# Optimization experiments

Hardware: AMD Instinct MI355X
Metric: run time of the kernel (lower is better)

The kernel has to match this reference:

```python
import jax, jax.numpy as jnp
import numpy as np

B, S, H, I, E, K = 2, 512, 512, 1024, 64, 4


def setup_inputs() -> dict:
    key = jax.random.key(0)
    ks = jax.random.split(key, 16)
    scale = jnp.float32(0.02)

    def w(k, shape):
        return jax.random.normal(k, shape, dtype=jnp.float32) * scale

    return {
        "x": jax.random.normal(ks[0], (B, S, H), dtype=jnp.float32),
        "router_w": w(ks[1], (E, H)),
        "router_b": w(ks[2], (E,)),
        "expert_biases": jnp.zeros((E,), dtype=jnp.float32),
        "sw1": w(ks[3], (I, H)), "sb1": w(ks[4], (I,)),
        "sw2": w(ks[5], (H, I)), "sb2": w(ks[6], (H,)),
        "sw3": w(ks[7], (I, H)), "sb3": w(ks[8], (I,)),
        "w1": w(ks[9], (E, I, H)), "b1": w(ks[10], (E, I)),
        "w2": w(ks[11], (E, H, I)), "b2": w(ks[12], (E, H)),
        "w3": w(ks[13], (E, I, H)), "b3": w(ks[14], (E, I)),
        "top_k": K,
    }


def _ffn(x, w1, b1, w2, b2, w3, b3):
    return (jax.nn.silu(x @ w1.T + b1) * (x @ w3.T + b3)) @ w2.T + b2


def reference(x, router_w, router_b, expert_biases,
              sw1, sb1, sw2, sb2, sw3, sb3,
              w1, b1, w2, b2, w3, b3, top_k):
    Bx, Sx, Hx = x.shape
    Ex = router_w.shape[0]

    # Router: logits [B,S,E]; top-k selection uses bias-adjusted logits,
    # but gates come from the ORIGINAL (unbiased) logits.
    logits = x @ router_w.T + router_b
    _, idx = jax.lax.top_k(logits + expert_biases, top_k)  # [B,S,K] int32
    orig = jnp.take_along_axis(logits, idx, axis=-1)       # [B,S,K]
    scores = jax.nn.sigmoid(orig)
    gates = scores / jnp.maximum(jnp.sum(scores, axis=-1, keepdims=True), 1e-12)

    # Shared expert(s): num_shared_experts == 1, divided by 1.
    shared = _ffn(x, sw1, sb1, sw2, sb2, sw3, sb3)

    # Combine gates into a dense per-token per-expert gate matrix [T,E].
    xf = x.reshape(-1, Hx)                 # [T,H]
    T = xf.shape[0]
    tok = jnp.arange(T)[:, None]
    gate_full = jnp.zeros((T, Ex), x.dtype).at[tok, idx.reshape(T, top_k)].add(
        gates.reshape(T, top_k))

    # Routed experts: each expert FFN over all tokens, gated combine.
    # (Mathematically identical to the original masked-dense loop: the mask
    #  zeroes both inputs and gates of unassigned tokens.)
    def body(acc, p):
        ew1, eb1, ew2, eb2, ew3, eb3, g = p
        y = _ffn(xf, ew1, eb1, ew2, eb2, ew3, eb3)  # [T,H]
        return acc + g[:, None] * y, None

    acc, _ = jax.lax.scan(body, jnp.zeros_like(xf),
                          (w1, b1, w2, b2, w3, b3, gate_full.T))

    return shared + acc.reshape(x.shape)
```

## Files before the change

### kernel.cpp

```cpp
#include <hip/hip_runtime.h>
#include <math.h>

#define T_    1024
#define H_    512
#define I_    1024
#define E_    64
#define K_    4
#define NPAIR (T_*K_)
#define NENT  (NPAIR + T_)

#define BM 128
#define BN 64
#define BKS 64
#define MAXWORK 160
#define NT1 (H_/BKS)
#define NT2 (I_/BKS)

typedef float  f32x4  __attribute__((ext_vector_type(4)));
typedef short  bf16x8 __attribute__((ext_vector_type(8)));

__device__ __forceinline__ ushort f2bf(float f) {
    uint u = __float_as_uint(f);
    u += 0x7fffu + ((u >> 16) & 1u);
    return (ushort)(u >> 16);
}
__device__ __forceinline__ bf16x8 cvt8(f32x4 a, f32x4 b) {
    bf16x8 r;
    r[0] = (short)f2bf(a[0]); r[1] = (short)f2bf(a[1]);
    r[2] = (short)f2bf(a[2]); r[3] = (short)f2bf(a[3]);
    r[4] = (short)f2bf(b[0]); r[5] = (short)f2bf(b[1]);
    r[6] = (short)f2bf(b[2]); r[7] = (short)f2bf(b[3]);
    return r;
}

__device__ __forceinline__ void gload16(const void* g, void* lds) {
    __builtin_amdgcn_global_load_lds(
        (const __attribute__((address_space(1))) unsigned int*)g,
        (__attribute__((address_space(3))) unsigned int*)lds, 16, 0, 0);
}

__global__ __launch_bounds__(256) void x_cvt(const float* __restrict__ x,
                                             ushort* __restrict__ xb)
{
    const int i = blockIdx.x*256 + threadIdx.x;
    float4 v = reinterpret_cast<const float4*>(x)[i];
    reinterpret_cast<ushort4*>(xb)[i] =
        make_ushort4(f2bf(v.x), f2bf(v.y), f2bf(v.z), f2bf(v.w));
}

__global__ __launch_bounds__(64) void moe_router(
    const float* __restrict__ x, const float* __restrict__ rw,
    const float* __restrict__ rb, const float* __restrict__ eb,
    int* __restrict__ idx_out, float* __restrict__ gate_out)
{
    const int t = blockIdx.x;
    const int lane = threadIdx.x;
    __shared__ float xs[H_];
    __shared__ float lg[E_];
    __shared__ float bs[E_];
    for (int i = lane; i < H_; i += 64) xs[i] = x[(size_t)t*H_ + i];
    bs[lane] = eb[lane];
    __syncthreads();
    float acc = 0.f;
    const float* wrow = rw + (size_t)lane*H_;
    for (int k = 0; k < H_; k += 4) {
        float4 w4 = *reinterpret_cast<const float4*>(wrow + k);
        acc = fmaf(xs[k+0], w4.x, acc);
        acc = fmaf(xs[k+1], w4.y, acc);
        acc = fmaf(xs[k+2], w4.z, acc);
        acc = fmaf(xs[k+3], w4.w, acc);
    }
    lg[lane] = acc + rb[lane];
    __syncthreads();
    if (lane == 0) {
        unsigned long long used = 0ull;
        int sel[K_]; float orig[K_];
        for (int k = 0; k < K_; ++k) {
            float best = -INFINITY; int bi = 0;
            for (int e = 0; e < E_; ++e) {
                if (used & (1ull << e)) continue;
                float v = lg[e] + bs[e];
                if (v > best) { best = v; bi = e; }
            }
            used |= (1ull << bi);
            sel[k] = bi; orig[k] = lg[bi];
        }
        float s[K_]; float sum = 0.f;
        for (int k = 0; k < K_; ++k) { s[k] = 1.f/(1.f + __expf(-orig[k])); sum += s[k]; }
        sum = fmaxf(sum, 1e-12f);
        for (int k = 0; k < K_; ++k) {
            idx_out[t*K_ + k] = sel[k];
            gate_out[t*K_ + k] = s[k] / sum;
        }
    }
}

__global__ __launch_bounds__(256) void moe_build(
    const int* __restrict__ idx, const float* __restrict__ gates,
    int* __restrict__ cnts, int* __restrict__ offs,
    int* __restrict__ entry_token, float* __restrict__ entry_gate,
    int* __restrict__ pair_pos,
    int* __restrict__ blk_e, int* __restrict__ blk_ro, int* __restrict__ nwork)
{
    __shared__ int c[E_];
    __shared__ int run[E_];
    const int tid = threadIdx.x;
    if (tid < E_) c[tid] = 0;
    __syncthreads();
    for (int p = tid; p < NPAIR; p += 256) atomicAdd(&c[idx[p]], 1);
    __syncthreads();
    if (tid == 0) {
        int o = 0;
        for (int e = 0; e < E_; ++e) { run[e] = o; offs[e] = o; cnts[e] = c[e]; o += c[e]; }
        offs[E_] = NPAIR;
        cnts[E_] = T_;
        int nb = 0;
        for (int e = 0; e <= E_; ++e) {
            int n = (e < E_) ? c[e] : T_;
            for (int ro = 0; ro < n; ro += BM) { blk_e[nb] = e; blk_ro[nb] = ro; ++nb; }
        }
        nwork[0] = nb;
    }
    __syncthreads();
    for (int p = tid; p < NPAIR; p += 256) {
        int e = idx[p];
        int pos = atomicAdd(&run[e], 1);
        entry_token[pos] = p / K_;
        entry_gate[pos]  = gates[p];
        pair_pos[p]      = pos;
    }
    for (int t = tid; t < T_; t += 256) {
        entry_token[NPAIR + t] = t;
        entry_gate[NPAIR + t]  = 1.0f;
    }
}

__global__ __launch_bounds__(256, 3) void moe_stage1(
    const ushort* __restrict__ xbf,
    const float* __restrict__ w1, const float* __restrict__ b1,
    const float* __restrict__ w3, const float* __restrict__ b3,
    const float* __restrict__ sw1, const float* __restrict__ sb1,
    const float* __restrict__ sw3, const float* __restrict__ sb3,
    const int* __restrict__ cnts, const int* __restrict__ offs,
    const int* __restrict__ entry_token,
    const int* __restrict__ blk_e, const int* __restrict__ blk_ro,
    const int* __restrict__ nwork,
    ushort* __restrict__ h1buf)
{
    const int w = blockIdx.x;
    if (w >= nwork[0]) return;
    const int e  = blk_e[w];
    const int ro = blk_ro[w];
    const int itile = blockIdx.y;
    const int n = cnts[e];
    const int off = offs[e];
    const int rows = min(BM, n - ro);
    const float* W1 = (e < E_) ? (w1 + (size_t)e*I_*H_) : sw1;
    const float* W3 = (e < E_) ? (w3 + (size_t)e*I_*H_) : sw3;
    const float* B1 = (e < E_) ? (b1 + (size_t)e*I_) : sb1;
    const float* B3 = (e < E_) ? (b3 + (size_t)e*I_) : sb3;

    __shared__ __align__(16) ushort XL [BM*BKS];
    __shared__ __align__(16) float  W1L[BN*BKS];
    __shared__ __align__(16) float  W3L[BN*BKS];

    const int tid  = threadIdx.x;
    const int lane = tid & 63;
    const int wid  = tid >> 6;
    const int wm   = wid >> 1;
    const int wn   = wid & 1;
    const int l15  = lane & 15;
    const int lg   = lane >> 4;

    const ushort* xsrc[4];
    const float* w1src[4];
    const float* w3src[4];
    #pragma unroll
    for (int i = 0; i < 4; ++i) {
        const int j = wid*4 + i;
        const int rX = j*8 + (lane >> 3);
        const int cX = (lane & 7) ^ (rX & 7);
        xsrc[i] = xbf + (size_t)entry_token[off + ro + rX]*H_ + cX*8;
        const int rW = j*4 + (lane >> 4);
        const int c32 = ((lane & 15) >> 1) ^ (rW & 7);
        const int colW = c32*8 + (lane & 1)*4;
        w1src[i] = W1 + (size_t)(itile*BN + rW)*H_ + colW;
        w3src[i] = W3 + (size_t)(itile*BN + rW)*H_ + colW;
    }

    f32x4 acc1[4][2] = {};
    f32x4 acc3[4][2] = {};

    for (int t = 0; t < NT1; ++t) {
        const int kc = t * BKS;
        #pragma unroll
        for (int i = 0; i < 4; ++i)
            gload16(xsrc[i] + kc, (char*)XL + (wid*4 + i)*1024);
        #pragma unroll
        for (int i = 0; i < 4; ++i)
            gload16(w1src[i] + kc, (char*)W1L + (wid*4 + i)*1024);
        #pragma unroll
        for (int i = 0; i < 4; ++i)
            gload16(w3src[i] + kc, (char*)W3L + (wid*4 + i)*1024);
        __syncthreads();
        #pragma unroll
        for (int s = 0; s < 2; ++s) {
            bf16x8 a[4];
            #pragma unroll
            for (int fm = 0; fm < 4; ++fm) {
                const int rr = wm*64 + fm*16 + l15;
                a[fm] = *reinterpret_cast<const bf16x8*>(
                    (const char*)XL + rr*128 + (((s*4 + lg) ^ (rr & 7)) << 4));
            }
            bf16x8 b1f[2], b3f[2];
            #pragma unroll
            for (int fn = 0; fn < 2; ++fn) {
                const int rw = wn*32 + fn*16 + l15;
                const int cw = ((s*4 + lg) ^ (rw & 7)) << 5;
                const char* p1 = (const char*)W1L + rw*256 + cw;
                b1f[fn] = cvt8(*reinterpret_cast<const f32x4*>(p1),
                               *reinterpret_cast<const f32x4*>(p1 + 16));
                const char* p3 = (const char*)W3L + rw*256 + cw;
                b3f[fn] = cvt8(*reinterpret_cast<const f32x4*>(p3),
                               *reinterpret_cast<const f32x4*>(p3 + 16));
            }
            #pragma unroll
            for (int fm = 0; fm < 4; ++fm) {
                #pragma unroll
                for (int fn = 0; fn < 2; ++fn) {
                    acc1[fm][fn] = __builtin_amdgcn_mfma_f32_16x16x32_bf16(a[fm], b1f[fn], acc1[fm][fn], 0, 0, 0);
                    acc3[fm][fn] = __builtin_amdgcn_mfma_f32_16x16x32_bf16(a[fm], b3f[fn], acc3[fm][fn], 0, 0, 0);
                }
            }
        }
        __syncthreads();
    }

    #pragma unroll
    for (int fm = 0; fm < 4; ++fm) {
        #pragma unroll
        for (int fn = 0; fn < 2; ++fn) {
            const int col = itile*BN + wn*32 + fn*16 + l15;
            const float bv1 = B1[col];
            const float bv3 = B3[col];
            #pragma unroll
            for (int j = 0; j < 4; ++j) {
                const int rl = wm*64 + fm*16 + lg*4 + j;
                if (rl < rows) {
                    float z1 = acc1[fm][fn][j] + bv1;
                    float z3 = acc3[fm][fn][j] + bv3;
                    float h = z1 / (1.f + __expf(-z1)) * z3;
                    h1buf[(size_t)(off+ro+rl)*I_ + col] = f2bf(h);
                }
            }
        }
    }
}

__global__ __launch_bounds__(256, 4) void moe_stage2(
    const ushort* __restrict__ h1buf,
    const float* __restrict__ w2, const float* __restrict__ b2,
    const float* __restrict__ sw2, const float* __restrict__ sb2,
    const int* __restrict__ cnts, const int* __restrict__ offs,
    const float* __restrict__ entry_gate,
    const int* __restrict__ blk_e, const int* __restrict__ blk_ro,
    const int* __restrict__ nwork,
    float* __restrict__ ybuf)
{
    const int w = blockIdx.x;
    if (w >= nwork[0]) return;
    const int e  = blk_e[w];
    const int ro = blk_ro[w];
    const int htile = blockIdx.y;
    const int n = cnts[e];
    const int off = offs[e];
    const int rows = min(BM, n - ro);
    const float* W2 = (e < E_) ? (w2 + (size_t)e*H_*I_) : sw2;
    const float* B2 = (e < E_) ? (b2 + (size_t)e*H_) : sb2;

    __shared__ __align__(16) ushort HL [BM*BKS];
    __shared__ __align__(16) float  W2L[BN*BKS];

    const int tid  = threadIdx.x;
    const int lane = tid & 63;
    const int wid  = tid >> 6;
    const int wm   = wid >> 1;
    const int wn   = wid & 1;
    const int l15  = lane & 15;
    const int lg   = lane >> 4;

    const ushort* hsrc[4];
    const float*  wsrc[4];
    #pragma unroll
    for (int i = 0; i < 4; ++i) {
        const int j = wid*4 + i;
        const int rH = j*8 + (lane >> 3);
        const int cH = (lane & 7) ^ (rH & 7);
        hsrc[i] = h1buf + (size_t)(off + ro + rH)*I_ + cH*8;
        const int rW = j*4 + (lane >> 4);
        const int c32 = ((lane & 15) >> 1) ^ (rW & 7);
        wsrc[i] = W2 + (size_t)(htile*BN + rW)*I_ + c32*8 + (lane & 1)*4;
    }

    f32x4 acc[4][2] = {};

    for (int t = 0; t < NT2; ++t) {
        const int kc = t * BKS;
        #pragma unroll
        for (int i = 0; i < 4; ++i)
            gload16(hsrc[i] + kc, (char*)HL + (wid*4 + i)*1024);
        #pragma unroll
        for (int i = 0; i < 4; ++i)
            gload16(wsrc[i] + kc, (char*)W2L + (wid*4 + i)*1024);
        __syncthreads();
        #pragma unroll
        for (int s = 0; s < 2; ++s) {
            bf16x8 a[4];
            #pragma unroll
            for (int fm = 0; fm < 4; ++fm) {
                const int rr = wm*64 + fm*16 + l15;
                a[fm] = *reinterpret_cast<const bf16x8*>(
                    (const char*)HL + rr*128 + (((s*4 + lg) ^ (rr & 7)) << 4));
            }
            bf16x8 bf[2];
            #pragma unroll
            for (int fn = 0; fn < 2; ++fn) {
                const int rw = wn*32 + fn*16 + l15;
                const char* p = (const char*)W2L + rw*256 + (((s*4 + lg) ^ (rw & 7)) << 5);
                bf[fn] = cvt8(*reinterpret_cast<const f32x4*>(p),
                              *reinterpret_cast<const f32x4*>(p + 16));
            }
            #pragma unroll
            for (int fm = 0; fm < 4; ++fm) {
                #pragma unroll
                for (int fn = 0; fn < 2; ++fn) {
                    acc[fm][fn] = __builtin_amdgcn_mfma_f32_16x16x32_bf16(a[fm], bf[fn], acc[fm][fn], 0, 0, 0);
                }
            }
        }
        __syncthreads();
    }

    #pragma unroll
    for (int fm = 0; fm < 4; ++fm) {
        #pragma unroll
        for (int fn = 0; fn < 2; ++fn) {
            const int col = htile*BN + wn*32 + fn*16 + l15;
            const float bv = B2[col];
            #pragma unroll
            for (int j = 0; j < 4; ++j) {
                const int rl = wm*64 + fm*16 + lg*4 + j;
                if (rl < rows) {
                    const float g = entry_gate[off + ro + rl];
                    ybuf[(size_t)(off+ro+rl)*H_ + col] = (acc[fm][fn][j] + bv) * g;
                }
            }
        }
    }
}

__global__ __launch_bounds__(128) void moe_combine(
    const float* __restrict__ ybuf, const int* __restrict__ pair_pos,
    float* __restrict__ out)
{
    const int t = blockIdx.x;
    const int lane = threadIdx.x;
    const int h = lane * 4;
    const int p0 = pair_pos[t*K_+0], p1 = pair_pos[t*K_+1];
    const int p2 = pair_pos[t*K_+2], p3 = pair_pos[t*K_+3];
    float4 a  = *reinterpret_cast<const float4*>(ybuf + (size_t)(NPAIR+t)*H_ + h);
    float4 v0 = *reinterpret_cast<const float4*>(ybuf + (size_t)p0*H_ + h);
    float4 v1 = *reinterpret_cast<const float4*>(ybuf + (size_t)p1*H_ + h);
    float4 v2 = *reinterpret_cast<const float4*>(ybuf + (size_t)p2*H_ + h);
    float4 v3 = *reinterpret_cast<const float4*>(ybuf + (size_t)p3*H_ + h);
    float4 r;
    r.x = a.x + v0.x + v1.x + v2.x + v3.x;
    r.y = a.y + v0.y + v1.y + v2.y + v3.y;
    r.z = a.z + v0.z + v1.z + v2.z + v3.z;
    r.w = a.w + v0.w + v1.w + v2.w + v3.w;
    *reinterpret_cast<float4*>(out + (size_t)t*H_ + h) = r;
}

extern "C" void kernel_launch(void* const* d_in, const int* in_sizes, int n_in,
                              void* d_out, int out_size, void* d_ws, size_t ws_size,
                              hipStream_t stream)
{
    const float* x   = (const float*)d_in[0];
    const float* rw  = (const float*)d_in[1];
    const float* rb  = (const float*)d_in[2];
    const float* eb  = (const float*)d_in[3];
    const float* sw1 = (const float*)d_in[4];
    const float* sb1 = (const float*)d_in[5];
    const float* sw2 = (const float*)d_in[6];
    const float* sb2 = (const float*)d_in[7];
    const float* sw3 = (const float*)d_in[8];
    const float* sb3 = (const float*)d_in[9];
    const float* w1  = (const float*)d_in[10];
    const float* b1  = (const float*)d_in[11];
    const float* w2  = (const float*)d_in[12];
    const float* b2  = (const float*)d_in[13];
    const float* w3  = (const float*)d_in[14];
    const float* b3  = (const float*)d_in[15];
    float* out = (float*)d_out;

    char* p = (char*)d_ws;
    auto take = [&](size_t bytes) { char* q = p; p += (bytes + 255) & ~(size_t)255; return q; };
    int*    idxb  = (int*)   take((size_t)NPAIR*4);
    float*  gateb = (float*) take((size_t)NPAIR*4);
    int*    cnts  = (int*)   take((E_+1)*4);
    int*    offs  = (int*)   take((E_+1)*4);
    int*    etok  = (int*)   take((size_t)NENT*4);
    float*  egate = (float*) take((size_t)NENT*4);
    int*    ppos  = (int*)   take((size_t)NPAIR*4);
    int*    blk_e = (int*)   take((size_t)MAXWORK*4);
    int*    blk_ro= (int*)   take((size_t)MAXWORK*4);
    int*    nwork = (int*)   take(4);
    ushort* xbf   = (ushort*)take((size_t)T_*H_*2);
    ushort* h1buf = (ushort*)take((size_t)NENT*I_*2);
    float*  ybuf  = (float*) take((size_t)NENT*H_*4);

    x_cvt      <<<(T_*H_)/(256*4), 256, 0, stream>>>(x, xbf);
    moe_router <<<T_, 64, 0, stream>>>(x, rw, rb, eb, idxb, gateb);
    moe_build  <<<1, 256, 0, stream>>>(idxb, gateb, cnts, offs, etok, egate, ppos,
                                       blk_e, blk_ro, nwork);
    moe_stage1 <<<dim3(MAXWORK, I_/BN), 256, 0, stream>>>(xbf, w1, b1, w3, b3,
                                                          sw1, sb1, sw3, sb3,
                                                          cnts, offs, etok,
                                                          blk_e, blk_ro, nwork, h1buf);
    moe_stage2 <<<dim3(MAXWORK, H_/BN), 256, 0, stream>>>(h1buf, w2, b2, sw2, sb2,
                                                          cnts, offs, egate,
                                                          blk_e, blk_ro, nwork, ybuf);
    moe_combine<<<T_, 128, 0, stream>>>(ybuf, ppos, out);
}
```

Measured before the change: 201.7 us.

## Double-buffer LDS tiles in expert GEMMs with halved K-step and packed bf16 convert

Both expert GEMM kernels now keep two LDS buffers and issue the async global-to-LDS loads for the next K-step before computing on the current one. This lets memory latency overlap with the MFMAs instead of stalling at a barrier on every iteration. To keep LDS usage the same, the K-step is halved from 64 to 32, which doubles the number of iterations and barriers; the XOR swizzle and load addressing are rewritten for the narrower tile. The per-element software fp32-to-bf16 rounding is replaced with the hardware v_cvt_pk_bf16_f32 instruction, which cuts VALU work when converting the weight fragments.

```diff
diff --git a/kernel.cpp b/kernel.cpp
--- a/kernel.cpp
+++ b/kernel.cpp
@@ -11,26 +11,28 @@
 
 #define BM 128
 #define BN 64
-#define BKS 64
+#define BKS 32
 #define MAXWORK 160
 #define NT1 (H_/BKS)
 #define NT2 (I_/BKS)
 
 typedef float  f32x4  __attribute__((ext_vector_type(4)));
 typedef short  bf16x8 __attribute__((ext_vector_type(8)));
+
+#define STEP_SYNC() asm volatile("s_waitcnt vmcnt(0) lgkmcnt(0)\n\ts_barrier" ::: "memory")
 
 __device__ __forceinline__ ushort f2bf(float f) {
     uint u = __float_as_uint(f);
     u += 0x7fffu + ((u >> 16) & 1u);
     return (ushort)(u >> 16);
 }
-__device__ __forceinline__ bf16x8 cvt8(f32x4 a, f32x4 b) {
-    bf16x8 r;
-    r[0] = (short)f2bf(a[0]); r[1] = (short)f2bf(a[1]);
-    r[2] = (short)f2bf(a[2]); r[3] = (short)f2bf(a[3]);
-    r[4] = (short)f2bf(b[0]); r[5] = (short)f2bf(b[1]);
-    r[6] = (short)f2bf(b[2]); r[7] = (short)f2bf(b[3]);
-    return r;
+__device__ __forceinline__ bf16x8 cvt8pk(f32x4 a, f32x4 b) {
+    union { uint u[4]; bf16x8 v; } r;
+    asm("v_cvt_pk_bf16_f32 %0, %1, %2" : "=v"(r.u[0]) : "v"(a[0]), "v"(a[1]));
+    asm("v_cvt_pk_bf16_f32 %0, %1, %2" : "=v"(r.u[1]) : "v"(a[2]), "v"(a[3]));
+    asm("v_cvt_pk_bf16_f32 %0, %1, %2" : "=v"(r.u[2]) : "v"(b[0]), "v"(b[1]));
+    asm("v_cvt_pk_bf16_f32 %0, %1, %2" : "=v"(r.u[3]) : "v"(b[2]), "v"(b[3]));
+    return r.v;
 }
 
 __device__ __forceinline__ void gload16(const void* g, void* lds) {
@@ -160,9 +162,9 @@
     const float* B1 = (e < E_) ? (b1 + (size_t)e*I_) : sb1;
     const float* B3 = (e < E_) ? (b3 + (size_t)e*I_) : sb3;
 
-    __shared__ __align__(16) ushort XL [BM*BKS];
-    __shared__ __align__(16) float  W1L[BN*BKS];
-    __shared__ __align__(16) float  W3L[BN*BKS];
+    __shared__ __align__(16) ushort XL [2][BM*BKS];
+    __shared__ __align__(16) float  W1L[2][BN*BKS];
+    __shared__ __align__(16) float  W3L[2][BN*BKS];
 
     const int tid  = threadIdx.x;
     const int lane = tid & 63;
@@ -172,69 +174,73 @@
     const int l15  = lane & 15;
     const int lg   = lane >> 4;
 
-    const ushort* xsrc[4];
-    const float* w1src[4];
-    const float* w3src[4];
+    const ushort* xsrc[2];
+    const float* w1src[2];
+    const float* w3src[2];
     #pragma unroll
-    for (int i = 0; i < 4; ++i) {
-        const int j = wid*4 + i;
-        const int rX = j*8 + (lane >> 3);
-        const int cX = (lane & 7) ^ (rX & 7);
+    for (int i = 0; i < 2; ++i) {
+        const int j = wid*2 + i;
+        const int rX = j*16 + (lane >> 2);
+        const int cX = (lane & 3) ^ ((rX >> 1) & 3);
         xsrc[i] = xbf + (size_t)entry_token[off + ro + rX]*H_ + cX*8;
-        const int rW = j*4 + (lane >> 4);
-        const int c32 = ((lane & 15) >> 1) ^ (rW & 7);
-        const int colW = c32*8 + (lane & 1)*4;
-        w1src[i] = W1 + (size_t)(itile*BN + rW)*H_ + colW;
-        w3src[i] = W3 + (size_t)(itile*BN + rW)*H_ + colW;
+        const int rW = j*8 + (lane >> 3);
+        const int cW = (lane & 7) ^ (rW & 7);
+        w1src[i] = W1 + (size_t)(itile*BN + rW)*H_ + cW*4;
+        w3src[i] = W3 + (size_t)(itile*BN + rW)*H_ + cW*4;
     }
 
     f32x4 acc1[4][2] = {};
     f32x4 acc3[4][2] = {};
 
+    #define STAGE1(t, buf)                                                        \
+        do {                                                                      \
+            const int kc_ = (t) * BKS;                                            \
+            _Pragma("unroll")                                                     \
+            for (int i_ = 0; i_ < 2; ++i_) {                                      \
+                gload16(xsrc[i_] + kc_,  (char*)&XL [buf][0] + (wid*2 + i_)*1024);\
+                gload16(w1src[i_] + kc_, (char*)&W1L[buf][0] + (wid*2 + i_)*1024);\
+                gload16(w3src[i_] + kc_, (char*)&W3L[buf][0] + (wid*2 + i_)*1024);\
+            }                                                                     \
+        } while (0)
+
+    STAGE1(0, 0);
+    STEP_SYNC();
+
     for (int t = 0; t < NT1; ++t) {
-        const int kc = t * BKS;
-        #pragma unroll
-        for (int i = 0; i < 4; ++i)
-            gload16(xsrc[i] + kc, (char*)XL + (wid*4 + i)*1024);
-        #pragma unroll
-        for (int i = 0; i < 4; ++i)
-            gload16(w1src[i] + kc, (char*)W1L + (wid*4 + i)*1024);
-        #pragma unroll
-        for (int i = 0; i < 4; ++i)
-            gload16(w3src[i] + kc, (char*)W3L + (wid*4 + i)*1024);
-        __syncthreads();
-        #pragma unroll
-        for (int s = 0; s < 2; ++s) {
-            bf16x8 a[4];
-            #pragma unroll
-            for (int fm = 0; fm < 4; ++fm) {
-                const int rr = wm*64 + fm*16 + l15;
-                a[fm] = *reinterpret_cast<const bf16x8*>(
-                    (const char*)XL + rr*128 + (((s*4 + lg) ^ (rr & 7)) << 4));
-            }
-            bf16x8 b1f[2], b3f[2];
+        const int cur = t & 1;
+        if (t + 1 < NT1) STAGE1(t + 1, cur ^ 1);
+        __builtin_amdgcn_sched_barrier(0);
+        bf16x8 a[4];
+        #pragma unroll
+        for (int fm = 0; fm < 4; ++fm) {
+            const int rr = wm*64 + fm*16 + l15;
+            a[fm] = *reinterpret_cast<const bf16x8*>(
+                (const char*)&XL[cur][0] + rr*64 + ((lg ^ ((rr >> 1) & 3)) << 4));
+        }
+        bf16x8 b1f[2], b3f[2];
+        #pragma unroll
+        for (int fn = 0; fn < 2; ++fn) {
+            const int rw = wn*32 + fn*16 + l15;
+            const int c0 = ((2*lg)     ^ (rw & 7)) << 4;
+            const int c1 = ((2*lg + 1) ^ (rw & 7)) << 4;
+            const char* p1 = (const char*)&W1L[cur][0] + rw*128;
+            b1f[fn] = cvt8pk(*reinterpret_cast<const f32x4*>(p1 + c0),
+                             *reinterpret_cast<const f32x4*>(p1 + c1));
+            const char* p3 = (const char*)&W3L[cur][0] + rw*128;
+            b3f[fn] = cvt8pk(*reinterpret_cast<const f32x4*>(p3 + c0),
+                             *reinterpret_cast<const f32x4*>(p3 + c1));
+        }
+        #pragma unroll
+        for (int fm = 0; fm < 4; ++fm) {
             #pragma unroll
             for (int fn = 0; fn < 2; ++fn) {
-                const int rw = wn*32 + fn*16 + l15;
-                const int cw = ((s*4 + lg) ^ (rw & 7)) << 5;
-                const char* p1 = (const char*)W1L + rw*256 + cw;
-                b1f[fn] = cvt8(*reinterpret_cast<const f32x4*>(p1),
-                               *reinterpret_cast<const f32x4*>(p1 + 16));
-                const char* p3 = (const char*)W3L + rw*256 + cw;
-                b3f[fn] = cvt8(*reinterpret_cast<const f32x4*>(p3),
-                               *reinterpret_cast<const f32x4*>(p3 + 16));
+                acc1[fm][fn] = __builtin_amdgcn_mfma_f32_16x16x32_bf16(a[fm], b1f[fn], acc1[fm][fn], 0, 0, 0);
+                acc3[fm][fn] = __builtin_amdgcn_mfma_f32_16x16x32_bf16(a[fm], b3f[fn], acc3[fm][fn], 0, 0, 0);
             }
-            #pragma unroll
-            for (int fm = 0; fm < 4; ++fm) {
-                #pragma unroll
-                for (int fn = 0; fn < 2; ++fn) {
-                    acc1[fm][fn] = __builtin_amdgcn_mfma_f32_16x16x32_bf16(a[fm], b1f[fn], acc1[fm][fn], 0, 0, 0);
-                    acc3[fm][fn] = __builtin_amdgcn_mfma_f32_16x16x32_bf16(a[fm], b3f[fn], acc3[fm][fn], 0, 0, 0);
-                }
-            }
-        }
-        __syncthreads();
-    }
+        }
+        if (t + 1 < NT1) STEP_SYNC();
+    }
+    #undef STAGE1
 
     #pragma unroll
     for (int fm = 0; fm < 4; ++fm) {
@@ -278,8 +284,8 @@
     const float* W2 = (e < E_) ? (w2 + (size_t)e*H_*I_) : sw2;
     const float* B2 = (e < E_) ? (b2 + (size_t)e*H_) : sb2;
 
-    __shared__ __align__(16) ushort HL [BM*BKS];
-    __shared__ __align__(16) float  W2L[BN*BKS];
+    __shared__ __align__(16) ushort HL [2][BM*BKS];
+    __shared__ __align__(16) float  W2L[2][BN*BKS];
 
     const int tid  = threadIdx.x;
     const int lane = tid & 63;
@@ -289,57 +295,65 @@
     const int l15  = lane & 15;
     const int lg   = lane >> 4;
 
-    const ushort* hsrc[4];
-    const float*  wsrc[4];
+    const ushort* hsrc[2];
+    const float*  wsrc[2];
     #pragma unroll
-    for (int i = 0; i < 4; ++i) {
-        const int j = wid*4 + i;
-        const int rH = j*8 + (lane >> 3);
-        const int cH = (lane & 7) ^ (rH & 7);
+    for (int i = 0; i < 2; ++i) {
+        const int j = wid*2 + i;
+        const int rH = j*16 + (lane >> 2);
+        const int cH = (lane & 3) ^ ((rH >> 1) & 3);
         hsrc[i] = h1buf + (size_t)(off + ro + rH)*I_ + cH*8;
-        const int rW = j*4 + (lane >> 4);
-        const int c32 = ((lane & 15) >> 1) ^ (rW & 7);
-        wsrc[i] = W2 + (size_t)(htile*BN + rW)*I_ + c32*8 + (lane & 1)*4;
+        const int rW = j*8 + (lane >> 3);
+        const int cW = (lane & 7) ^ (rW & 7);
+        wsrc[i] = W2 + (size_t)(htile*BN + rW)*I_ + cW*4;
     }
 
     f32x4 acc[4][2] = {};
 
+    #define STAGE2(t, buf)                                                        \
+        do {                                                                      \
+            const int kc_ = (t) * BKS;                                            \
+            _Pragma("unroll")                                                     \
+            for (int i_ = 0; i_ < 2; ++i_) {                                      \
+                gload16(hsrc[i_] + kc_, (char*)&HL [buf][0] + (wid*2 + i_)*1024); \
+                gload16(wsrc[i_] + kc_, (char*)&W2L[buf][0] + (wid*2 + i_)*1024); \
+            }                                                                     \
+        } while (0)
+
+    STAGE2(0, 0);
+    STEP_SYNC();
+
     for (int t = 0; t < NT2; ++t) {
-        const int kc = t * BKS;
-        #pragma unroll
-        for (int i = 0; i < 4; ++i)
-            gload16(hsrc[i] + kc, (char*)HL + (wid*4 + i)*1024);
-        #pragma unroll
-        for (int i = 0; i < 4; ++i)
-            gload16(wsrc[i] + kc, (char*)W2L + (wid*4 + i)*1024);
-        __syncthreads();
-        #pragma unroll
-        for (int s = 0; s < 2; ++s) {
-            bf16x8 a[4];
-            #pragma unroll
-            for (int fm = 0; fm < 4; ++fm) {
-                const int rr = wm*64 + fm*16 + l15;
-                a[fm] = *reinterpret_cast<const bf16x8*>(
-                    (const char*)HL + rr*128 + (((s*4 + lg) ^ (rr & 7)) << 4));
-            }
-            bf16x8 bf[2];
+        const int cur = t & 1;
+        if (t + 1 < NT2) STAGE2(t + 1, cur ^ 1);
+        __builtin_amdgcn_sched_barrier(0);
+        bf16x8 a[4];
+        #pragma unroll
+        for (int fm = 0; fm < 4; ++fm) {
+            const int rr = wm*64 + fm*16 + l15;
+            a[fm] = *reinterpret_cast<const bf16x8*>(
+                (const char*)&HL[cur][0] + rr*64 + ((lg ^ ((rr >> 1) & 3)) << 4));
+        }
+        bf16x8 bf[2];
+        #pragma unroll
+        for (int fn = 0; fn < 2; ++fn) {
+            const int rw = wn*32 + fn*16 + l15;
+            const int c0 = ((2*lg)     ^ (rw & 7)) << 4;
+            const int c1 = ((2*lg + 1) ^ (rw & 7)) << 4;
+            const char* p = (const char*)&W2L[cur][0] + rw*128;
+            bf[fn] = cvt8pk(*reinterpret_cast<const f32x4*>(p + c0),
+                            *reinterpret_cast<const f32x4*>(p + c1));
+        }
+        #pragma unroll
+        for (int fm = 0; fm < 4; ++fm) {
             #pragma unroll
             for (int fn = 0; fn < 2; ++fn) {
-                const int rw = wn*32 + fn*16 + l15;
-                const char* p = (const char*)W2L + rw*256 + (((s*4 + lg) ^ (rw & 7)) << 5);
-                bf[fn] = cvt8(*reinterpret_cast<const f32x4*>(p),
-                              *reinterpret_cast<const f32x4*>(p + 16));
+                acc[fm][fn] = __builtin_amdgcn_mfma_f32_16x16x32_bf16(a[fm], bf[fn], acc[fm][fn], 0, 0, 0);
             }
-            #pragma unroll
-            for (int fm = 0; fm < 4; ++fm) {
-                #pragma unroll
-                for (int fn = 0; fn < 2; ++fn) {
-                    acc[fm][fn] = __builtin_amdgcn_mfma_f32_16x16x32_bf16(a[fm], bf[fn], acc[fm][fn], 0, 0, 0);
-                }
-            }
-        }
-        __syncthreads();
-    }
+        }
+        if (t + 1 < NT2) STEP_SYNC();
+    }
+    #undef STAGE2
 
     #pragma unroll
     for (int fm = 0; fm < 4; ++fm) {
```

New measurement: 216.7 us. 1.07x slower.
